# Optimization experiments

Hardware: AMD Instinct MI355X
Metric: run time of the kernel (lower is better)

The kernel has to match this reference:

```python
import jax, jax.numpy as jnp
import numpy as np

B, N, C = 2, 2048, 512
H = 8
HD = C // H


def _xavier(key, shape):
    fan_in, fan_out = shape[-1], shape[-2] if len(shape) > 1 else shape[-1]
    limit = float(np.sqrt(6.0 / (fan_in + fan_out)))
    return jax.random.uniform(key, shape, jnp.float32, -limit, limit)


def setup_inputs() -> dict:
    key = jax.random.key(0)
    ks = jax.random.split(key, 8)
    return {
        "x": jax.random.normal(ks[0], (B, N, C), jnp.float32),
        "pos_embedding": jax.random.normal(ks[1], (B, N, C), jnp.float32),
        "Wqkv": _xavier(ks[2], (3 * C, C)),      # nn.Linear(dim, 3*dim, bias=False)
        "Wpos": _xavier(ks[3], (C, C)),          # pos_proj, bias=False
        "u_bias": _xavier(ks[4], (H, HD)),
        "v_bias": _xavier(ks[5], (H, HD)),
        "Wproj": _xavier(ks[6], (C, C)),
        "bproj": jnp.zeros((C,), jnp.float32),
    }


def _relative_shift(ps):
    # ps: [B, H, N, M]
    b, h, n, m = ps.shape
    ps = jnp.pad(ps, ((0, 0), (0, 0), (0, 0), (1, 0)))  # zero column in front
    ps = ps.reshape(b, h, m + 1, n)[:, :, 1:, :]
    return ps.reshape(b, h, n, m)


def reference(x, pos_embedding, Wqkv, Wpos, u_bias, v_bias, Wproj, bproj):
    b, n, c = x.shape
    scale = HD ** -0.5
    qkv = (x @ Wqkv.T).reshape(b, n, 3, H, HD)
    q = qkv[:, :, 0].transpose(0, 2, 1, 3)  # [B,H,N,HD]
    k = qkv[:, :, 1].transpose(0, 2, 1, 3)
    v = qkv[:, :, 2].transpose(0, 2, 1, 3)
    pos = (pos_embedding @ Wpos.T).reshape(b, -1, H, HD)  # [B,M,H,HD]

    # content score: (q + u_bias) @ k^T -> [B,H,N,N]
    content = jnp.einsum("bhnd,bhmd->bhnm", q + u_bias[None, :, None, :], k)
    # pos score: (q + v_bias) @ pos^T -> [B,H,N,M]
    pos_score = jnp.einsum("bhnd,bmhd->bhnm", q + v_bias[None, :, None, :], pos)
    pos_score = _relative_shift(pos_score)

    attn = jax.nn.softmax((pos_score + content) * scale, axis=-1)
    out = jnp.einsum("bhnm,bhmd->bhnd", attn, v)
    out = out.transpose(0, 2, 1, 3).reshape(b, n, c)
    return out @ Wproj.T + bproj
```

## Files before the change

### kernel.cpp

```cpp
#include <hip/hip_runtime.h>

typedef __attribute__((ext_vector_type(8))) short bf16x8;
typedef __attribute__((ext_vector_type(4))) short bf16x4;
typedef __attribute__((ext_vector_type(4))) float f32x4;

__device__ __forceinline__ float bf2f(unsigned short u) {
  union { unsigned int i; float f; } c; c.i = ((unsigned int)u) << 16; return c.f;
}
__device__ __forceinline__ unsigned short f2bf(float x) {
  union { float f; unsigned int i; } c; c.f = x;
  return (unsigned short)((c.i + 0x7fffu + ((c.i >> 16) & 1u)) >> 16);
}
__device__ __forceinline__ unsigned int pk2(float a, float b) {
  return (unsigned int)f2bf(a) | ((unsigned int)f2bf(b) << 16);
}

__device__ __forceinline__ uint4 ld8f(const float* p) {
  const float4 a = *(const float4*)p;
  const float4 b = *(const float4*)(p + 4);
  uint4 r;
  r.x = (unsigned)f2bf(a.x) | ((unsigned)f2bf(a.y) << 16);
  r.y = (unsigned)f2bf(a.z) | ((unsigned)f2bf(a.w) << 16);
  r.z = (unsigned)f2bf(b.x) | ((unsigned)f2bf(b.y) << 16);
  r.w = (unsigned)f2bf(b.z) | ((unsigned)f2bf(b.w) << 16);
  return r;
}

__device__ __forceinline__ void gload16(const unsigned short* g, short* l) {
  __builtin_amdgcn_global_load_lds((const __attribute__((address_space(1))) void*)g,
                                   (__attribute__((address_space(3))) void*)l, 16, 0, 0);
}

__global__ __launch_bounds__(256) void k_cvt(const float* __restrict__ x,
    const float* __restrict__ pe, const float* __restrict__ wq,
    const float* __restrict__ wp, const float* __restrict__ wj,
    unsigned short* __restrict__ dst) {
  const long long i8 = ((long long)blockIdx.x * 256 + threadIdx.x) * 8;
  const float* src; long long off;
  if (i8 < 2097152)      { src = x;  off = i8; }
  else if (i8 < 4194304) { src = pe; off = i8 - 2097152; }
  else if (i8 < 4980736) { src = wq; off = i8 - 4194304; }
  else if (i8 < 5242880) { src = wp; off = i8 - 4980736; }
  else                   { src = wj; off = i8 - 5242880; }
  *(uint4*)&dst[i8] = ld8f(src + off);
}

__device__ __forceinline__ void gemm128_mainloop(const unsigned short* __restrict__ Arow,
                                                 const unsigned short* __restrict__ Wrow,
                                                 short* Asl, short* Wsl, f32x4 acc[4][4]) {
  const int tid = threadIdx.x, w = tid >> 6, lane = tid & 63, lm = lane & 15, lq = lane >> 4;
  const int wm = w >> 1, wn = w & 1;
  const int lrow = lane >> 3;
  const int gcol = (((lane & 7) ^ lrow) * 8);
#pragma unroll
  for (int mt = 0; mt < 4; ++mt)
#pragma unroll
    for (int nt = 0; nt < 4; ++nt) acc[mt][nt] = (f32x4){0.f, 0.f, 0.f, 0.f};
#pragma unroll 1
  for (int kc = 0; kc < 512; kc += 64) {
    __syncthreads();
#pragma unroll
    for (int ld = 0; ld < 4; ++ld) {
      const int rbase = w * 32 + ld * 8;
      gload16(&Arow[(size_t)(rbase + lrow) * 512 + kc + gcol], &Asl[rbase * 64]);
      gload16(&Wrow[(size_t)(rbase + lrow) * 512 + kc + gcol], &Wsl[rbase * 64]);
    }
    __syncthreads();
#pragma unroll
    for (int kk = 0; kk < 2; ++kk) {
      const int pcs = ((kk * 4 + lq) ^ (lm & 7)) * 8;
      bf16x8 af[4], bfr[4];
#pragma unroll
      for (int mt = 0; mt < 4; ++mt)
        af[mt] = *(const bf16x8*)&Asl[(wm * 64 + mt * 16 + lm) * 64 + pcs];
#pragma unroll
      for (int nt = 0; nt < 4; ++nt)
        bfr[nt] = *(const bf16x8*)&Wsl[(wn * 64 + nt * 16 + lm) * 64 + pcs];
#pragma unroll
      for (int mt = 0; mt < 4; ++mt)
#pragma unroll
        for (int nt = 0; nt < 4; ++nt)
          acc[mt][nt] = __builtin_amdgcn_mfma_f32_16x16x32_bf16(af[mt], bfr[nt], acc[mt][nt], 0, 0, 0);
    }
  }
}

__global__ __launch_bounds__(256) void k_gemm_qkvpos(const unsigned short* __restrict__ xb,
    const unsigned short* __restrict__ peb, const unsigned short* __restrict__ wqb,
    const unsigned short* __restrict__ wpb, const float* __restrict__ ub,
    const float* __restrict__ vb, unsigned short* __restrict__ qu,
    unsigned short* __restrict__ qv, unsigned short* __restrict__ kg,
    unsigned short* __restrict__ vg, unsigned short* __restrict__ pos) {
  __shared__ short Asl[128 * 64], Wsl[128 * 64];
  f32x4 acc[4][4];
  const int m0 = blockIdx.y * 128, cc0 = blockIdx.x * 128;
  const unsigned short* Arow = (cc0 < 1536 ? xb : peb) + (size_t)m0 * 512;
  const unsigned short* Wrow = (cc0 < 1536) ? (wqb + (size_t)cc0 * 512)
                                            : (wpb + (size_t)(cc0 - 1536) * 512);
  gemm128_mainloop(Arow, Wrow, Asl, Wsl, acc);
  const int tid = threadIdx.x, w = tid >> 6, lane = tid & 63, lm = lane & 15, lq = lane >> 4;
  const int wm = w >> 1, wn = w & 1;
#pragma unroll
  for (int nt = 0; nt < 4; ++nt) {
    const int cc = cc0 + wn * 64 + nt * 16 + lm;
    const int sec = cc >> 9, rem = cc & 511, h = rem >> 6, d = rem & 63;
#pragma unroll
    for (int mt = 0; mt < 4; ++mt) {
#pragma unroll
      for (int r = 0; r < 4; ++r) {
        const int m = m0 + wm * 64 + mt * 16 + lq * 4 + r;
        const int b = m >> 11, n = m & 2047;
        const size_t idx = ((size_t)(b * 8 + h) * 2048 + n) * 64 + d;
        const float val = acc[mt][nt][r];
        if (sec == 0) {
          qu[idx] = f2bf(val + ub[rem]);
          qv[idx] = f2bf(val + vb[rem]);
        } else if (sec == 1) {
          kg[idx] = f2bf(val);
        } else if (sec == 2) {
          vg[idx] = f2bf(val);
        } else {
          pos[idx] = f2bf(val);
        }
      }
    }
  }
}

__global__ __launch_bounds__(256) void k_transpose_v(const unsigned short* __restrict__ vg,
                                                     unsigned short* __restrict__ vt) {
  __shared__ short T[64][72];
  const int tid = threadIdx.x, bhid = blockIdx.y, n0 = blockIdx.x * 64;
#pragma unroll
  for (int s = 0; s < 2; ++s) {
    int u = tid + s * 256, row = u >> 3, c8 = (u & 7) * 8;
    *(uint4*)&T[row][c8] = *(const uint4*)&vg[((size_t)bhid * 2048 + n0 + row) * 64 + c8];
  }
  __syncthreads();
#pragma unroll
  for (int s = 0; s < 2; ++s) {
    int u = tid + s * 256, d = u >> 3, n8 = (u & 7) * 8;
    alignas(16) unsigned short tmp[8];
#pragma unroll
    for (int jj = 0; jj < 8; ++jj) tmp[jj] = (unsigned short)T[n8 + jj][d];
    *(uint4*)&vt[((size_t)bhid * 64 + d) * 2048 + n0 + n8] = *(const uint4*)tmp;
  }
}

__global__ __launch_bounds__(512, 4) void k_flash(const unsigned short* __restrict__ qu,
    const unsigned short* __restrict__ qv, const unsigned short* __restrict__ kg,
    const unsigned short* __restrict__ vt, const unsigned short* __restrict__ posg,
    unsigned short* __restrict__ og) {
  __shared__ short SB[23892];
  short* Ks = SB;
  short* Vs = SB + 4608;
  short* Pn = SB + 9216;
  short* T  = SB + 18432;
  float* Ored = (float*)SB;
  const int tid = threadIdx.x, w = tid >> 6, lane = tid & 63, lm = lane & 15, lq = lane >> 4;
  const int wk = w & 3;
  const int h  = w >> 2;
  const int sw = w >> 1;
  const int ph = w & 1;
  const int hw = blockIdx.x + 32 * blockIdx.y;
  const int xcd = hw & 7, idx = hw >> 3;
  const int bh = xcd * 2 + (idx & 1);
  const int i0 = (idx >> 1) * 64;
  const size_t bhs = (size_t)bh;
  const unsigned short* qub = qu + bhs * (2048 * 64);
  const unsigned short* qvb = qv + bhs * (2048 * 64);
  const unsigned short* pob = posg + bhs * (2048 * 64);
  bf16x8 au[2][2];
#pragma unroll
  for (int qt = 0; qt < 2; ++qt) {
    const int qs = h * 2 + qt;
    au[qt][0] = *(const bf16x8*)&qub[(size_t)(i0 + qs * 16 + lm) * 64 + lq * 8];
    au[qt][1] = *(const bf16x8*)&qub[(size_t)(i0 + qs * 16 + lm) * 64 + 32 + lq * 8];
  }
  const bf16x8 av0 = *(const bf16x8*)&qvb[(size_t)(i0 + sw * 16 + lm) * 64 + lq * 8];
  const bf16x8 av1 = *(const bf16x8*)&qvb[(size_t)(i0 + sw * 16 + lm) * 64 + 32 + lq * 8];
  const int rowe = min(i0 + 49 + lm, 2047);
  const bf16x8 ae0 = *(const bf16x8*)&qvb[(size_t)rowe * 64 + lq * 8];
  const bf16x8 ae1 = *(const bf16x8*)&qvb[(size_t)rowe * 64 + 32 + lq * 8];
  float lsum[2] = {0.f, 0.f};
  f32x4 oacc[2][4];
#pragma unroll
  for (int ii = 0; ii < 2; ++ii)
#pragma unroll
    for (int jj = 0; jj < 4; ++jj) oacc[ii][jj] = (f32x4){0.f, 0.f, 0.f, 0.f};
  const int krow = tid >> 3, kc8 = (tid & 7) * 8;
  const int pb0 = 1983 - i0;
  uint4 kr = *(const uint4*)&kg[(bhs * 2048 + krow) * 64 + kc8];
  uint4 vr = *(const uint4*)&vt[(bhs * 64 + krow) * 2048 + kc8];
  uint4 pr[2];
#pragma unroll
  for (int s = 0; s < 2; ++s) {
    int u = tid + s * 512, prow = u >> 3, c8 = (u & 7) * 8;
    int grow = (pb0 + prow + 4096) & 2047;
    pr[s] = *(const uint4*)&pob[(size_t)grow * 64 + c8];
  }
#pragma unroll 1
  for (int jt = 0; jt < 32; ++jt) {
    const int j0 = jt * 64;
    const int pb = pb0 + j0;
    __syncthreads();
    *(uint4*)&Ks[krow * 72 + kc8] = kr;
    *(uint4*)&Vs[krow * 72 + kc8] = vr;
    if (jt == 0) {
#pragma unroll
      for (int s = 0; s < 2; ++s) {
        int u = tid + s * 512, prow = u >> 3, c8 = (u & 7) * 8;
        int slot = (pb + prow) & 127;
        *(uint4*)&Pn[slot * 72 + c8] = pr[s];
      }
    } else {
      const int slot = (pb + 64 + krow) & 127;
      *(uint4*)&Pn[slot * 72 + kc8] = pr[0];
    }
    __syncthreads();
    if (jt < 31) {
      const int jn = j0 + 64;
      kr = *(const uint4*)&kg[(bhs * 2048 + jn + krow) * 64 + kc8];
      vr = *(const uint4*)&vt[(bhs * 64 + krow) * 2048 + jn + kc8];
      const int grow = (pb + 128 + krow + 4096) & 2047;
      pr[0] = *(const uint4*)&pob[(size_t)grow * 64 + kc8];
    }
    const bf16x8 k0 = *(const bf16x8*)&Ks[(wk * 16 + lm) * 72 + lq * 8];
    const bf16x8 k1 = *(const bf16x8*)&Ks[(wk * 16 + lm) * 72 + 32 + lq * 8];
    f32x4 cacc[2];
#pragma unroll
    for (int qt = 0; qt < 2; ++qt) {
      cacc[qt] = __builtin_amdgcn_mfma_f32_16x16x32_bf16(k0, au[qt][0], (f32x4){0.f,0.f,0.f,0.f}, 0, 0, 0);
      cacc[qt] = __builtin_amdgcn_mfma_f32_16x16x32_bf16(k1, au[qt][1], cacc[qt], 0, 0, 0);
    }
    const int sbase = 49 - sw * 16;
    if (ph == 0) {
#pragma unroll
      for (int ct = 0; ct < 3; ++ct) {
        const int slot = (pb + sbase + ct * 16 + lm) & 127;
        const bf16x8 b0 = *(const bf16x8*)&Pn[slot * 72 + lq * 8];
        const bf16x8 b1 = *(const bf16x8*)&Pn[slot * 72 + 32 + lq * 8];
        f32x4 t0 = __builtin_amdgcn_mfma_f32_16x16x32_bf16(b0, av0, (f32x4){0.f,0.f,0.f,0.f}, 0, 0, 0);
        t0 = __builtin_amdgcn_mfma_f32_16x16x32_bf16(b1, av1, t0, 0, 0, 0);
        uint2 pk; pk.x = pk2(t0[0], t0[1]); pk.y = pk2(t0[2], t0[3]);
        *(uint2*)&T[(sw * 16 + lm) * 84 + ct * 16 + lq * 4] = pk;
      }
    } else {
#pragma unroll
      for (int ct = 3; ct < 5; ++ct) {
        const int slot = (pb + sbase + ct * 16 + lm) & 127;
        const bf16x8 b0 = *(const bf16x8*)&Pn[slot * 72 + lq * 8];
        const bf16x8 b1 = *(const bf16x8*)&Pn[slot * 72 + 32 + lq * 8];
        f32x4 t0 = __builtin_amdgcn_mfma_f32_16x16x32_bf16(b0, av0, (f32x4){0.f,0.f,0.f,0.f}, 0, 0, 0);
        t0 = __builtin_amdgcn_mfma_f32_16x16x32_bf16(b1, av1, t0, 0, 0, 0);
        uint2 pk; pk.x = pk2(t0[0], t0[1]); pk.y = pk2(t0[2], t0[3]);
        *(uint2*)&T[(sw * 16 + lm) * 84 + ct * 16 + lq * 4] = pk;
      }
      {
        const int slot = (pb + sw * 16 + lm) & 127;
        const bf16x8 b0 = *(const bf16x8*)&Pn[slot * 72 + lq * 8];
        const bf16x8 b1 = *(const bf16x8*)&Pn[slot * 72 + 32 + lq * 8];
        f32x4 e0 = __builtin_amdgcn_mfma_f32_16x16x32_bf16(b0, ae0, (f32x4){0.f,0.f,0.f,0.f}, 0, 0, 0);
        e0 = __builtin_amdgcn_mfma_f32_16x16x32_bf16(b1, ae1, e0, 0, 0, 0);
        if (lm == 15) {
          uint2 pk; pk.x = pk2(e0[0], e0[1]); pk.y = pk2(e0[2], e0[3]);
          *(uint2*)&T[64 * 84 + sw * 16 + lq * 4] = pk;
        }
      }
    }
    __syncthreads();
    const int diag = i0 - j0;
    const int jl0 = wk * 16 + lq * 4;
    bf16x4 pf[2];
    if (diag >= 64 || diag <= -128) {
      const int du = (diag <= -128) ? 1 : 0;
      const int rm = lm + du;
#pragma unroll
      for (int qt = 0; qt < 2; ++qt) {
        const int rowa = (h * 2 + qt) * 16 + rm;
        const int base = (rowa == 64) ? (64 * 84 + jl0)
                                      : (rowa * 84 + 15 + jl0 - (rm & 15));
#pragma unroll
        for (int r = 0; r < 4; ++r) {
          const float pv = bf2f((unsigned short)T[base + r]);
          const float p = exp2f((cacc[qt][r] + pv) * 0.18033688f);
          lsum[qt] += p;
          pf[qt][r] = (short)f2bf(p);
        }
      }
    } else {
#pragma unroll
      for (int qt = 0; qt < 2; ++qt) {
        const int qs = h * 2 + qt;
#pragma unroll
        for (int r = 0; r < 4; ++r) {
          const int jl = jl0 + r;
          const int d = (j0 - i0) + jl - (qs * 16 + lm);
          float pv;
          if (d == 1) {
            pv = 0.f;
          } else {
            const int rm2 = lm + ((d > 1) ? 1 : 0);
            const int rowa = qs * 16 + rm2;
            const int base = (rowa == 64) ? (64 * 84 + jl)
                                          : (rowa * 84 + 15 + jl - (rm2 & 15));
            pv = bf2f((unsigned short)T[base]);
          }
          const float p = exp2f((cacc[qt][r] + pv) * 0.18033688f);
          lsum[qt] += p;
          pf[qt][r] = (short)f2bf(p);
        }
      }
    }
#pragma unroll
    for (int dt = 0; dt < 4; ++dt) {
      const bf16x4 vf = *(const bf16x4*)&Vs[(dt * 16 + lm) * 72 + wk * 16 + lq * 4];
      oacc[0][dt] = __builtin_amdgcn_mfma_f32_16x16x16bf16_1k(pf[0], vf, oacc[0][dt], 0, 0, 0);
      oacc[1][dt] = __builtin_amdgcn_mfma_f32_16x16x16bf16_1k(pf[1], vf, oacc[1][dt], 0, 0, 0);
    }
  }
#pragma unroll
  for (int qt = 0; qt < 2; ++qt) {
    lsum[qt] += __shfl_xor(lsum[qt], 16, 64);
    lsum[qt] += __shfl_xor(lsum[qt], 32, 64);
  }
  __syncthreads();
  if (wk == 0) {
#pragma unroll
    for (int qt = 0; qt < 2; ++qt) {
      const int qc = (h * 2 + qt) * 16;
#pragma unroll
      for (int dt = 0; dt < 4; ++dt)
        *(f32x4*)&Ored[(dt * 16 + lm) * 68 + qc + lq * 4] = oacc[qt][dt];
      if (lq == 0) Ored[64 * 68 + qc + lm] = lsum[qt];
    }
  }
  __syncthreads();
#pragma unroll 1
  for (int r = 1; r < 4; ++r) {
    if (wk == r) {
#pragma unroll
      for (int qt = 0; qt < 2; ++qt) {
        const int qc = (h * 2 + qt) * 16;
#pragma unroll
        for (int dt = 0; dt < 4; ++dt) {
          f32x4 o = *(const f32x4*)&Ored[(dt * 16 + lm) * 68 + qc + lq * 4];
          o += oacc[qt][dt];
          *(f32x4*)&Ored[(dt * 16 + lm) * 68 + qc + lq * 4] = o;
        }
        if (lq == 0) Ored[64 * 68 + qc + lm] += lsum[qt];
      }
    }
    __syncthreads();
  }
  if (w < 4) {
    const int b = bh >> 3, hh = bh & 7;
    const f32x4 lv = *(const f32x4*)&Ored[64 * 68 + w * 16 + lq * 4];
    f32x4 inv;
#pragma unroll
    for (int r = 0; r < 4; ++r) inv[r] = 1.f / lv[r];
#pragma unroll
    for (int dt = 0; dt < 4; ++dt) {
      const f32x4 o = *(const f32x4*)&Ored[(dt * 16 + lm) * 68 + w * 16 + lq * 4];
#pragma unroll
      for (int r = 0; r < 4; ++r)
        og[((size_t)b * 2048 + i0 + w * 16 + lq * 4 + r) * 512 + hh * 64 + dt * 16 + lm] =
            f2bf(o[r] * inv[r]);
    }
  }
}

__global__ __launch_bounds__(256) void k_gemm_proj(const unsigned short* __restrict__ og,
    const unsigned short* __restrict__ wjb, const float* __restrict__ bproj,
    float* __restrict__ out) {
  __shared__ short Asl[128 * 64], Wsl[128 * 64];
  f32x4 acc[4][4];
  const int m0 = blockIdx.y * 128, cc0 = blockIdx.x * 128;
  gemm128_mainloop(og + (size_t)m0 * 512, wjb + (size_t)cc0 * 512, Asl, Wsl, acc);
  const int tid = threadIdx.x, w = tid >> 6, lane = tid & 63, lm = lane & 15, lq = lane >> 4;
  const int wm = w >> 1, wn = w & 1;
#pragma unroll
  for (int nt = 0; nt < 4; ++nt) {
    const int cc = cc0 + wn * 64 + nt * 16 + lm;
    const float bias = bproj[cc];
#pragma unroll
    for (int mt = 0; mt < 4; ++mt) {
#pragma unroll
      for (int r = 0; r < 4; ++r) {
        const int m = m0 + wm * 64 + mt * 16 + lq * 4 + r;
        out[(size_t)m * 512 + cc] = acc[mt][nt][r] + bias;
      }
    }
  }
}

extern "C" void kernel_launch(void* const* d_in, const int* in_sizes, int n_in,
                              void* d_out, int out_size, void* d_ws, size_t ws_size,
                              hipStream_t stream) {
  const float* x     = (const float*)d_in[0];
  const float* pe    = (const float*)d_in[1];
  const float* wqkv  = (const float*)d_in[2];
  const float* wpos  = (const float*)d_in[3];
  const float* ub    = (const float*)d_in[4];
  const float* vb    = (const float*)d_in[5];
  const float* wproj = (const float*)d_in[6];
  const float* bproj = (const float*)d_in[7];
  float* out = (float*)d_out;
  unsigned short* ws = (unsigned short*)d_ws;

  const size_t SZ = (size_t)2 * 8 * 2048 * 64;
  unsigned short* qu   = ws;
  unsigned short* qv   = qu + SZ;
  unsigned short* kg   = qv + SZ;
  unsigned short* vg   = kg + SZ;
  unsigned short* vt   = vg + SZ;
  unsigned short* pos  = vt + SZ;
  unsigned short* og   = pos + SZ;
  unsigned short* cvtb = og + SZ;
  unsigned short* xb   = cvtb;
  unsigned short* peb  = cvtb + 2097152;
  unsigned short* wqb  = cvtb + 4194304;
  unsigned short* wpb  = cvtb + 4980736;
  unsigned short* wjb  = cvtb + 5242880;

  dim3 blk(256);
  hipLaunchKernelGGL(k_cvt,         dim3(2688),   blk, 0, stream, x, pe, wqkv, wpos, wproj, cvtb);
  hipLaunchKernelGGL(k_gemm_qkvpos, dim3(16, 32), blk, 0, stream,
                     xb, peb, wqb, wpb, ub, vb, qu, qv, kg, vg, pos);
  hipLaunchKernelGGL(k_transpose_v, dim3(32, 16), blk, 0, stream, vg, vt);
  hipLaunchKernelGGL(k_flash,       dim3(32, 16), dim3(512), 0, stream, qu, qv, kg, vt, pos, og);
  hipLaunchKernelGGL(k_gemm_proj,   dim3(4, 32),  blk, 0, stream, og, wjb, bproj, out);
}
```

Measured before the change: 219.6 us.

## Read K, V and pos operands directly from global memory, double-buffer T

Removes the shared-memory staging of K, V and the pos ring buffer in the flash kernel. MFMA operands are now loaded straight from global memory (relying on L1/L2), and the T scratch tile is double-buffered, which drops two barriers per iteration. The smaller LDS footprint lets launch bounds rise to 6 blocks per CU. The risk is more global traffic and latency per iteration, redundant loads of the same K/V data across warps, and register pressure under the tighter occupancy bound.

```diff
diff --git a/kernel.cpp b/kernel.cpp
--- a/kernel.cpp
+++ b/kernel.cpp
@@ -147,15 +147,11 @@
   }
 }
 
-__global__ __launch_bounds__(512, 4) void k_flash(const unsigned short* __restrict__ qu,
+__global__ __launch_bounds__(512, 6) void k_flash(const unsigned short* __restrict__ qu,
     const unsigned short* __restrict__ qv, const unsigned short* __restrict__ kg,
     const unsigned short* __restrict__ vt, const unsigned short* __restrict__ posg,
     unsigned short* __restrict__ og) {
-  __shared__ short SB[23892];
-  short* Ks = SB;
-  short* Vs = SB + 4608;
-  short* Pn = SB + 9216;
-  short* T  = SB + 18432;
+  __shared__ short SB[2 * 5460];
   float* Ored = (float*)SB;
   const int tid = threadIdx.x, w = tid >> 6, lane = tid & 63, lm = lane & 15, lq = lane >> 4;
   const int wk = w & 3;
@@ -170,6 +166,8 @@
   const unsigned short* qub = qu + bhs * (2048 * 64);
   const unsigned short* qvb = qv + bhs * (2048 * 64);
   const unsigned short* pob = posg + bhs * (2048 * 64);
+  const unsigned short* kgb = kg + bhs * (2048 * 64);
+  const unsigned short* vtb = vt + bhs * (2048 * 64);
   bf16x8 au[2][2];
 #pragma unroll
   for (int qt = 0; qt < 2; ++qt) {
@@ -188,45 +186,14 @@
   for (int ii = 0; ii < 2; ++ii)
 #pragma unroll
     for (int jj = 0; jj < 4; ++jj) oacc[ii][jj] = (f32x4){0.f, 0.f, 0.f, 0.f};
-  const int krow = tid >> 3, kc8 = (tid & 7) * 8;
   const int pb0 = 1983 - i0;
-  uint4 kr = *(const uint4*)&kg[(bhs * 2048 + krow) * 64 + kc8];
-  uint4 vr = *(const uint4*)&vt[(bhs * 64 + krow) * 2048 + kc8];
-  uint4 pr[2];
-#pragma unroll
-  for (int s = 0; s < 2; ++s) {
-    int u = tid + s * 512, prow = u >> 3, c8 = (u & 7) * 8;
-    int grow = (pb0 + prow + 4096) & 2047;
-    pr[s] = *(const uint4*)&pob[(size_t)grow * 64 + c8];
-  }
 #pragma unroll 1
   for (int jt = 0; jt < 32; ++jt) {
     const int j0 = jt * 64;
     const int pb = pb0 + j0;
-    __syncthreads();
-    *(uint4*)&Ks[krow * 72 + kc8] = kr;
-    *(uint4*)&Vs[krow * 72 + kc8] = vr;
-    if (jt == 0) {
-#pragma unroll
-      for (int s = 0; s < 2; ++s) {
-        int u = tid + s * 512, prow = u >> 3, c8 = (u & 7) * 8;
-        int slot = (pb + prow) & 127;
-        *(uint4*)&Pn[slot * 72 + c8] = pr[s];
-      }
-    } else {
-      const int slot = (pb + 64 + krow) & 127;
-      *(uint4*)&Pn[slot * 72 + kc8] = pr[0];
-    }
-    __syncthreads();
-    if (jt < 31) {
-      const int jn = j0 + 64;
-      kr = *(const uint4*)&kg[(bhs * 2048 + jn + krow) * 64 + kc8];
-      vr = *(const uint4*)&vt[(bhs * 64 + krow) * 2048 + jn + kc8];
-      const int grow = (pb + 128 + krow + 4096) & 2047;
-      pr[0] = *(const uint4*)&pob[(size_t)grow * 64 + kc8];
-    }
-    const bf16x8 k0 = *(const bf16x8*)&Ks[(wk * 16 + lm) * 72 + lq * 8];
-    const bf16x8 k1 = *(const bf16x8*)&Ks[(wk * 16 + lm) * 72 + 32 + lq * 8];
+    short* T = SB + (jt & 1) * 5460;
+    const bf16x8 k0 = *(const bf16x8*)&kgb[(size_t)(j0 + wk * 16 + lm) * 64 + lq * 8];
+    const bf16x8 k1 = *(const bf16x8*)&kgb[(size_t)(j0 + wk * 16 + lm) * 64 + 32 + lq * 8];
     f32x4 cacc[2];
 #pragma unroll
     for (int qt = 0; qt < 2; ++qt) {
@@ -237,9 +204,9 @@
     if (ph == 0) {
 #pragma unroll
       for (int ct = 0; ct < 3; ++ct) {
-        const int slot = (pb + sbase + ct * 16 + lm) & 127;
-        const bf16x8 b0 = *(const bf16x8*)&Pn[slot * 72 + lq * 8];
-        const bf16x8 b1 = *(const bf16x8*)&Pn[slot * 72 + 32 + lq * 8];
+        const int grow = (pb + sbase + ct * 16 + lm + 4096) & 2047;
+        const bf16x8 b0 = *(const bf16x8*)&pob[(size_t)grow * 64 + lq * 8];
+        const bf16x8 b1 = *(const bf16x8*)&pob[(size_t)grow * 64 + 32 + lq * 8];
         f32x4 t0 = __builtin_amdgcn_mfma_f32_16x16x32_bf16(b0, av0, (f32x4){0.f,0.f,0.f,0.f}, 0, 0, 0);
         t0 = __builtin_amdgcn_mfma_f32_16x16x32_bf16(b1, av1, t0, 0, 0, 0);
         uint2 pk; pk.x = pk2(t0[0], t0[1]); pk.y = pk2(t0[2], t0[3]);
@@ -248,18 +215,18 @@
     } else {
 #pragma unroll
       for (int ct = 3; ct < 5; ++ct) {
-        const int slot = (pb + sbase + ct * 16 + lm) & 127;
-        const bf16x8 b0 = *(const bf16x8*)&Pn[slot * 72 + lq * 8];
-        const bf16x8 b1 = *(const bf16x8*)&Pn[slot * 72 + 32 + lq * 8];
+        const int grow = (pb + sbase + ct * 16 + lm + 4096) & 2047;
+        const bf16x8 b0 = *(const bf16x8*)&pob[(size_t)grow * 64 + lq * 8];
+        const bf16x8 b1 = *(const bf16x8*)&pob[(size_t)grow * 64 + 32 + lq * 8];
         f32x4 t0 = __builtin_amdgcn_mfma_f32_16x16x32_bf16(b0, av0, (f32x4){0.f,0.f,0.f,0.f}, 0, 0, 0);
         t0 = __builtin_amdgcn_mfma_f32_16x16x32_bf16(b1, av1, t0, 0, 0, 0);
         uint2 pk; pk.x = pk2(t0[0], t0[1]); pk.y = pk2(t0[2], t0[3]);
         *(uint2*)&T[(sw * 16 + lm) * 84 + ct * 16 + lq * 4] = pk;
       }
       {
-        const int slot = (pb + sw * 16 + lm) & 127;
-        const bf16x8 b0 = *(const bf16x8*)&Pn[slot * 72 + lq * 8];
-        const bf16x8 b1 = *(const bf16x8*)&Pn[slot * 72 + 32 + lq * 8];
+        const int grow = (pb + sw * 16 + lm + 4096) & 2047;
+        const bf16x8 b0 = *(const bf16x8*)&pob[(size_t)grow * 64 + lq * 8];
+        const bf16x8 b1 = *(const bf16x8*)&pob[(size_t)grow * 64 + 32 + lq * 8];
         f32x4 e0 = __builtin_amdgcn_mfma_f32_16x16x32_bf16(b0, ae0, (f32x4){0.f,0.f,0.f,0.f}, 0, 0, 0);
         e0 = __builtin_amdgcn_mfma_f32_16x16x32_bf16(b1, ae1, e0, 0, 0, 0);
         if (lm == 15) {
@@ -314,7 +281,7 @@
     }
 #pragma unroll
     for (int dt = 0; dt < 4; ++dt) {
-      const bf16x4 vf = *(const bf16x4*)&Vs[(dt * 16 + lm) * 72 + wk * 16 + lq * 4];
+      const bf16x4 vf = *(const bf16x4*)&vtb[(size_t)(dt * 16 + lm) * 2048 + j0 + wk * 16 + lq * 4];
       oacc[0][dt] = __builtin_amdgcn_mfma_f32_16x16x16bf16_1k(pf[0], vf, oacc[0][dt], 0, 0, 0);
       oacc[1][dt] = __builtin_amdgcn_mfma_f32_16x16x16bf16_1k(pf[1], vf, oacc[1][dt], 0, 0, 0);
     }
```

New measurement: 407.0 us. +85.3%, slower.

## Stage QKV GEMM epilogue through LDS and fuse V transpose into it

Applied to the files above, without the earlier changes.

The QKV/pos GEMM epilogue now writes each 128x128 tile into shared memory and then emits 16-byte coalesced stores, replacing the scattered 2-byte per-element global stores. For the V section, the epilogue writes the transposed layout straight from LDS, so the separate transpose kernel and the intermediate vg buffer are removed. This cuts one launch and a full round trip of V through global memory. In exchange it adds extra LDS traffic and barriers in the epilogue, and the q section runs two staging passes.

```diff
diff --git a/kernel.cpp b/kernel.cpp
--- a/kernel.cpp
+++ b/kernel.cpp
@@ -85,65 +85,85 @@
   }
 }
 
+__device__ __forceinline__ void epi_rows(const f32x4 acc[4][4], const float* __restrict__ bias,
+                                         short* TT, unsigned short* __restrict__ dst,
+                                         int m0, int cc0) {
+  const int tid = threadIdx.x, w = tid >> 6, lane = tid & 63, lm = lane & 15, lq = lane >> 4;
+  const int wm = w >> 1, wn = w & 1;
+  __syncthreads();
+#pragma unroll
+  for (int mt = 0; mt < 4; ++mt)
+#pragma unroll
+    for (int nt = 0; nt < 4; ++nt) {
+      const int ccl = wn * 64 + nt * 16 + lm;
+      const float bb = bias ? bias[(cc0 + ccl) & 511] : 0.f;
+#pragma unroll
+      for (int r = 0; r < 4; ++r)
+        TT[(wm * 64 + mt * 16 + lq * 4 + r) * 130 + ccl] = (short)f2bf(acc[mt][nt][r] + bb);
+    }
+  __syncthreads();
+#pragma unroll
+  for (int rr = 0; rr < 8; ++rr) {
+    const int ml = rr * 16 + (tid >> 4), ccl = (tid & 15) * 8;
+    const uint4 v = *(const uint4*)&TT[ml * 130 + ccl];
+    const int m = m0 + ml, b = m >> 11, n = m & 2047;
+    const int cc = cc0 + ccl, hh = (cc >> 6) & 7, d = cc & 63;
+    *(uint4*)&dst[((size_t)(b * 8 + hh) * 2048 + n) * 64 + d] = v;
+  }
+}
+
+__device__ __forceinline__ void epi_cols(const f32x4 acc[4][4], short* TT,
+                                         unsigned short* __restrict__ vt,
+                                         int m0, int cc0) {
+  const int tid = threadIdx.x, w = tid >> 6, lane = tid & 63, lm = lane & 15, lq = lane >> 4;
+  const int wm = w >> 1, wn = w & 1;
+  __syncthreads();
+#pragma unroll
+  for (int mt = 0; mt < 4; ++mt)
+#pragma unroll
+    for (int nt = 0; nt < 4; ++nt) {
+      const int ccl = wn * 64 + nt * 16 + lm;
+#pragma unroll
+      for (int r = 0; r < 4; ++r)
+        TT[(wm * 64 + mt * 16 + lq * 4 + r) * 130 + ccl] = (short)f2bf(acc[mt][nt][r]);
+    }
+  __syncthreads();
+  const int b = m0 >> 11;
+#pragma unroll
+  for (int ss = 0; ss < 8; ++ss) {
+    const int ccl = ss * 16 + (tid >> 4), mch = (tid & 15) * 8;
+    alignas(16) unsigned short tmp[8];
+#pragma unroll
+    for (int j = 0; j < 8; ++j) tmp[j] = (unsigned short)TT[(mch + j) * 130 + ccl];
+    const int cc = cc0 + ccl, hh = (cc >> 6) & 7, d = cc & 63;
+    const int n = (m0 & 2047) + mch;
+    *(uint4*)&vt[((size_t)(b * 8 + hh) * 64 + d) * 2048 + n] = *(const uint4*)tmp;
+  }
+}
+
 __global__ __launch_bounds__(256) void k_gemm_qkvpos(const unsigned short* __restrict__ xb,
     const unsigned short* __restrict__ peb, const unsigned short* __restrict__ wqb,
     const unsigned short* __restrict__ wpb, const float* __restrict__ ub,
     const float* __restrict__ vb, unsigned short* __restrict__ qu,
     unsigned short* __restrict__ qv, unsigned short* __restrict__ kg,
-    unsigned short* __restrict__ vg, unsigned short* __restrict__ pos) {
-  __shared__ short Asl[128 * 64], Wsl[128 * 64];
+    unsigned short* __restrict__ vt, unsigned short* __restrict__ pos) {
+  __shared__ short SB[16640];
   f32x4 acc[4][4];
   const int m0 = blockIdx.y * 128, cc0 = blockIdx.x * 128;
   const unsigned short* Arow = (cc0 < 1536 ? xb : peb) + (size_t)m0 * 512;
   const unsigned short* Wrow = (cc0 < 1536) ? (wqb + (size_t)cc0 * 512)
                                             : (wpb + (size_t)(cc0 - 1536) * 512);
-  gemm128_mainloop(Arow, Wrow, Asl, Wsl, acc);
-  const int tid = threadIdx.x, w = tid >> 6, lane = tid & 63, lm = lane & 15, lq = lane >> 4;
-  const int wm = w >> 1, wn = w & 1;
-#pragma unroll
-  for (int nt = 0; nt < 4; ++nt) {
-    const int cc = cc0 + wn * 64 + nt * 16 + lm;
-    const int sec = cc >> 9, rem = cc & 511, h = rem >> 6, d = rem & 63;
-#pragma unroll
-    for (int mt = 0; mt < 4; ++mt) {
-#pragma unroll
-      for (int r = 0; r < 4; ++r) {
-        const int m = m0 + wm * 64 + mt * 16 + lq * 4 + r;
-        const int b = m >> 11, n = m & 2047;
-        const size_t idx = ((size_t)(b * 8 + h) * 2048 + n) * 64 + d;
-        const float val = acc[mt][nt][r];
-        if (sec == 0) {
-          qu[idx] = f2bf(val + ub[rem]);
-          qv[idx] = f2bf(val + vb[rem]);
-        } else if (sec == 1) {
-          kg[idx] = f2bf(val);
-        } else if (sec == 2) {
-          vg[idx] = f2bf(val);
-        } else {
-          pos[idx] = f2bf(val);
-        }
-      }
-    }
-  }
-}
-
-__global__ __launch_bounds__(256) void k_transpose_v(const unsigned short* __restrict__ vg,
-                                                     unsigned short* __restrict__ vt) {
-  __shared__ short T[64][72];
-  const int tid = threadIdx.x, bhid = blockIdx.y, n0 = blockIdx.x * 64;
-#pragma unroll
-  for (int s = 0; s < 2; ++s) {
-    int u = tid + s * 256, row = u >> 3, c8 = (u & 7) * 8;
-    *(uint4*)&T[row][c8] = *(const uint4*)&vg[((size_t)bhid * 2048 + n0 + row) * 64 + c8];
-  }
-  __syncthreads();
-#pragma unroll
-  for (int s = 0; s < 2; ++s) {
-    int u = tid + s * 256, d = u >> 3, n8 = (u & 7) * 8;
-    alignas(16) unsigned short tmp[8];
-#pragma unroll
-    for (int jj = 0; jj < 8; ++jj) tmp[jj] = (unsigned short)T[n8 + jj][d];
-    *(uint4*)&vt[((size_t)bhid * 64 + d) * 2048 + n0 + n8] = *(const uint4*)tmp;
+  gemm128_mainloop(Arow, Wrow, SB, SB + 8192, acc);
+  const int sec = cc0 >> 9;
+  if (sec == 0) {
+    epi_rows(acc, ub, SB, qu, m0, cc0);
+    epi_rows(acc, vb, SB, qv, m0, cc0);
+  } else if (sec == 1) {
+    epi_rows(acc, nullptr, SB, kg, m0, cc0);
+  } else if (sec == 2) {
+    epi_cols(acc, SB, vt, m0, cc0);
+  } else {
+    epi_rows(acc, nullptr, SB, pos, m0, cc0);
   }
 }
 
@@ -412,8 +432,7 @@
   unsigned short* qu   = ws;
   unsigned short* qv   = qu + SZ;
   unsigned short* kg   = qv + SZ;
-  unsigned short* vg   = kg + SZ;
-  unsigned short* vt   = vg + SZ;
+  unsigned short* vt   = kg + SZ;
   unsigned short* pos  = vt + SZ;
   unsigned short* og   = pos + SZ;
   unsigned short* cvtb = og + SZ;
@@ -426,8 +445,7 @@
   dim3 blk(256);
   hipLaunchKernelGGL(k_cvt,         dim3(2688),   blk, 0, stream, x, pe, wqkv, wpos, wproj, cvtb);
   hipLaunchKernelGGL(k_gemm_qkvpos, dim3(16, 32), blk, 0, stream,
-                     xb, peb, wqb, wpb, ub, vb, qu, qv, kg, vg, pos);
-  hipLaunchKernelGGL(k_transpose_v, dim3(32, 16), blk, 0, stream, vg, vt);
+                     xb, peb, wqb, wpb, ub, vb, qu, qv, kg, vt, pos);
   hipLaunchKernelGGL(k_flash,       dim3(32, 16), dim3(512), 0, stream, qu, qv, kg, vt, pos, og);
   hipLaunchKernelGGL(k_gemm_proj,   dim3(4, 32),  blk, 0, stream, og, wjb, bproj, out);
 }
```

After: 213.8 us (median of 2 runs). -2.7%, faster.
